# Optimization experiments

Hardware: AMD Instinct MI355X
Metric: run time of the kernel (lower is better)

Reference implementation:

```python
import jax, jax.numpy as jnp
import numpy as np

B, C, H, W = 16, 512, 32, 32
CQ = C // 8  # 64
EPS = 1e-5


def _conv1x1(x, Wt, b=None):
    # x: (B,C,H,W), Wt: (O,C) -> (B,O,H,W)
    y = jnp.einsum('bchw,oc->bohw', x, Wt)
    if b is not None:
        y = y + b[None, :, None, None]
    return y


def setup_inputs() -> dict:
    key = jax.random.key(0)
    ks = jax.random.split(key, 12)
    s = 0.02
    return {
        'rgb':    jax.random.normal(ks[0], (B, C, H, W), jnp.float32),
        'depth':  jax.random.normal(ks[1], (B, C, H, W), jnp.float32),
        'Wq_rgb': jax.random.normal(ks[2], (CQ, C), jnp.float32) * s,
        'bq_rgb': jnp.zeros((CQ,), jnp.float32),
        'Wk_dep': jax.random.normal(ks[3], (CQ, C), jnp.float32) * s,
        'bk_dep': jnp.zeros((CQ,), jnp.float32),
        'Wv_dep': jax.random.normal(ks[4], (C, C), jnp.float32) * s,
        'bv_dep': jnp.zeros((C,), jnp.float32),
        'Wq_dep': jax.random.normal(ks[5], (CQ, C), jnp.float32) * s,
        'bq_dep': jnp.zeros((CQ,), jnp.float32),
        'Wk_rgb': jax.random.normal(ks[6], (CQ, C), jnp.float32) * s,
        'bk_rgb': jnp.zeros((CQ,), jnp.float32),
        'Wv_rgb': jax.random.normal(ks[7], (C, C), jnp.float32) * s,
        'bv_rgb': jnp.zeros((C,), jnp.float32),
        'W_fuse': jax.random.normal(ks[8], (C, 2 * C), jnp.float32) * s,
        'gamma':  jnp.ones((C,), jnp.float32),
        'beta':   jnp.zeros((C,), jnp.float32),
    }


def reference(rgb, depth, Wq_rgb, bq_rgb, Wk_dep, bk_dep, Wv_dep, bv_dep,
              Wq_dep, bq_dep, Wk_rgb, bk_rgb, Wv_rgb, bv_rgb, W_fuse, gamma, beta):
    b, c, h, w = rgb.shape
    hw = h * w
    scale = jnp.asarray(c, rgb.dtype) ** 0.5  # note: full C, as in source

    # RGB attends to depth
    q = _conv1x1(rgb, Wq_rgb, bq_rgb).reshape(b, -1, hw).transpose(0, 2, 1)   # (B,HW,CQ)
    k = _conv1x1(depth, Wk_dep, bk_dep).reshape(b, -1, hw)                    # (B,CQ,HW)
    v = _conv1x1(depth, Wv_dep, bv_dep).reshape(b, -1, hw).transpose(0, 2, 1) # (B,HW,C)
    attn = jax.nn.softmax(jnp.einsum('bnd,bdm->bnm', q, k) / scale, axis=-1)
    rgb_att = jnp.einsum('bnm,bmc->bnc', attn, v).transpose(0, 2, 1).reshape(b, c, h, w)

    # Depth attends to RGB
    q2 = _conv1x1(depth, Wq_dep, bq_dep).reshape(b, -1, hw).transpose(0, 2, 1)
    k2 = _conv1x1(rgb, Wk_rgb, bk_rgb).reshape(b, -1, hw)
    v2 = _conv1x1(rgb, Wv_rgb, bv_rgb).reshape(b, -1, hw).transpose(0, 2, 1)
    attn2 = jax.nn.softmax(jnp.einsum('bnd,bdm->bnm', q2, k2) / scale, axis=-1)
    dep_att = jnp.einsum('bnm,bmc->bnc', attn2, v2).transpose(0, 2, 1).reshape(b, c, h, w)

    cat = jnp.concatenate([rgb_att, dep_att], axis=1)      # (B,2C,H,W)
    fused = jnp.einsum('bchw,oc->bohw', cat, W_fuse)        # 1x1 conv, no bias

    # BatchNorm2d in training mode (batch statistics, biased variance)
    mean = fused.mean(axis=(0, 2, 3))
    var = fused.var(axis=(0, 2, 3))
    normed = (fused - mean[None, :, None, None]) * jax.lax.rsqrt(var + EPS)[None, :, None, None]
    out = normed * gamma[None, :, None, None] + beta[None, :, None, None]
    return jax.nn.relu(out)
```

## Files before the change

### kernel.cpp

```cpp
#include <hip/hip_runtime.h>
#include <math.h>

#define NB 16
#define CC 512
#define CQ 64
#define HWN 1024

typedef float4 f4;
typedef __bf16 bf16x8 __attribute__((ext_vector_type(8)));
typedef float f32x4 __attribute__((ext_vector_type(4)));
typedef __attribute__((ext_vector_type(8))) unsigned short ushort8v;

__device__ __forceinline__ unsigned short f2bf(float f) {
    unsigned int u = __float_as_uint(f);
    u = (u + 0x7fffu + ((u >> 16) & 1u)) >> 16;
    return (unsigned short)u;
}
__device__ __forceinline__ float bf2f(unsigned short u) {
    return __uint_as_float(((unsigned int)u) << 16);
}

__device__ __forceinline__ void gload16(const unsigned short* g, unsigned short* l) {
    __builtin_amdgcn_global_load_lds(
        (const __attribute__((address_space(1))) unsigned int*)g,
        (__attribute__((address_space(3))) unsigned int*)l,
        16, 0, 0);
}

template<int BM, int BN, int BIAS, bool OBF16, int ZSH>
__global__ __launch_bounds__(256)
void mfma_g(const unsigned short* __restrict__ A, long sAlo, long sAhi, int lda,
            const unsigned short* __restrict__ B, long sBlo, long sBhi, int ldb,
            const float* __restrict__ bias, long sBiasHi,
            void* __restrict__ Cout, long sClo, long sChi, int ldc,
            int Ksize, float alpha)
{
    constexpr int MF = BM / 32;
    constexpr int NF = BN / 32;
    constexpr int CA = BM / 32;
    constexpr int CB = BN / 32;
    __shared__ unsigned short As[2][BM * 64];
    __shared__ unsigned short Bs[2][BN * 64];

    const int gx = gridDim.x, gy = gridDim.y;
    int f = blockIdx.x + gx * (blockIdx.y + gy * blockIdx.z);
    const int nwg = gx * gy * gridDim.z;
    f = (f & 7) * (nwg >> 3) + (f >> 3);
    const int bx = f % gx; const int t2 = f / gx;
    const int by = t2 % gy; const int bz = t2 / gy;

    const int zlo = ZSH ? (bz & ((1 << ZSH) - 1)) : 0;
    const int zhi = bz >> ZSH;

    const int t = threadIdx.x, lane = t & 63, wid = t >> 6;
    const int wm = (wid >> 1) * (BM / 2), wn = (wid & 1) * (BN / 2);
    const int m0 = by * BM, n0 = bx * BN;
    const unsigned short* Ab = A + (long)zlo * sAlo + (long)zhi * sAhi;
    const unsigned short* Bb = B + (long)zlo * sBlo + (long)zhi * sBhi;

    const int srow = lane >> 3;
    const int scol = ((lane & 7) ^ srow) << 3;
    const unsigned short* gA[CA]; const unsigned short* gB[CB];
    unsigned short* lA[CA]; unsigned short* lB[CB];
#pragma unroll
    for (int c = 0; c < CA; ++c) {
        const int seg = wid + 4 * c;
        gA[c] = Ab + (long)(m0 + seg * 8 + srow) * lda + scol;
        lA[c] = &As[0][seg * 512];
    }
#pragma unroll
    for (int c = 0; c < CB; ++c) {
        const int seg = wid + 4 * c;
        gB[c] = Bb + (long)(n0 + seg * 8 + srow) * ldb + scol;
        lB[c] = &Bs[0][seg * 512];
    }

    f32x4 acc[MF][NF] = {};
    const int l15 = lane & 15, slot = lane >> 4;

#pragma unroll
    for (int c = 0; c < CA; ++c) gload16(gA[c], lA[c]);
#pragma unroll
    for (int c = 0; c < CB; ++c) gload16(gB[c], lB[c]);
    __syncthreads();

    const int nt = Ksize >> 6;
    int cur = 0;
    for (int tt = 0; tt < nt; ++tt) {
        if (tt + 1 < nt) {
            const int ko = (tt + 1) << 6;
            const int nb = cur ^ 1;
#pragma unroll
            for (int c = 0; c < CA; ++c) gload16(gA[c] + ko, lA[c] + nb * (BM * 64));
#pragma unroll
            for (int c = 0; c < CB; ++c) gload16(gB[c] + ko, lB[c] + nb * (BN * 64));
        }
        bf16x8 alo[MF], ahi[MF], blo[NF], bhi[NF];
#pragma unroll
        for (int i = 0; i < MF; ++i) {
            const int r = wm + i * 16 + l15;
            alo[i] = *(const bf16x8*)&As[cur][r * 64 + ((slot ^ (r & 7)) << 3)];
            ahi[i] = *(const bf16x8*)&As[cur][r * 64 + (((slot + 4) ^ (r & 7)) << 3)];
        }
#pragma unroll
        for (int j = 0; j < NF; ++j) {
            const int r = wn + j * 16 + l15;
            blo[j] = *(const bf16x8*)&Bs[cur][r * 64 + ((slot ^ (r & 7)) << 3)];
            bhi[j] = *(const bf16x8*)&Bs[cur][r * 64 + (((slot + 4) ^ (r & 7)) << 3)];
        }
#pragma unroll
        for (int i = 0; i < MF; ++i)
#pragma unroll
            for (int j = 0; j < NF; ++j) {
                acc[i][j] = __builtin_amdgcn_mfma_f32_16x16x32_bf16(alo[i], blo[j], acc[i][j], 0, 0, 0);
                acc[i][j] = __builtin_amdgcn_mfma_f32_16x16x32_bf16(ahi[i], bhi[j], acc[i][j], 0, 0, 0);
            }
        __syncthreads();
        cur ^= 1;
    }

    unsigned short* C16 = (unsigned short*)Cout + (long)zlo * sClo + (long)zhi * sChi;
    float*          C32 = (float*)Cout + (long)zlo * sClo + (long)zhi * sChi;
    const float* biasb = (BIAS != 0) ? bias + (long)zhi * sBiasHi : nullptr;
    const int r0 = slot << 2;
#pragma unroll
    for (int i = 0; i < MF; ++i) {
#pragma unroll
        for (int r = 0; r < 4; ++r) {
            const int m = m0 + wm + i * 16 + r0 + r;
            const float brow = (BIAS == 1) ? biasb[m] : 0.0f;
#pragma unroll
            for (int j = 0; j < NF; ++j) {
                const int n = n0 + wn + j * 16 + l15;
                const float bb = (BIAS == 2) ? biasb[n] : brow;
                const float o = alpha * (acc[i][j][r] + bb);
                if (OBF16) C16[(long)m * ldc + n] = f2bf(o);
                else       C32[(long)m * ldc + n] = o;
            }
        }
    }
}

__global__ __launch_bounds__(256)
void attn_fused(const unsigned short* __restrict__ QK, unsigned short* __restrict__ Pcat)
{
    __shared__ unsigned short Ss[32][1024];
    const int t = threadIdx.x, lane = t & 63, w = t >> 6;
    const int bx = blockIdx.x, b = blockIdx.y, dir = blockIdx.z;
    const unsigned short* Q = QK + (long)(dir ? b : 16 + b) * 131072;
    const unsigned short* K = QK + (long)(dir ? 16 + b : b) * 131072 + 64;
    const int l15 = lane & 15, kg = (lane >> 4) << 3;

    const long mrow = bx * 32 + (w & 1) * 16 + l15;
    bf16x8 aq0 = *(const bf16x8*)&Q[mrow * 128 + kg];
    bf16x8 aq1 = *(const bf16x8*)&Q[mrow * 128 + 32 + kg];

    const int colbase = (w >> 1) * 512;
    const int rbase = (w & 1) * 16 + (lane >> 4) * 4;
    for (int c = 0; c < 4; ++c) {
        const int n0 = colbase + c * 128;
        bf16x8 bk0[8], bk1[8];
#pragma unroll
        for (int j = 0; j < 8; ++j) {
            const long krow = n0 + j * 16 + l15;
            bk0[j] = *(const bf16x8*)&K[krow * 128 + kg];
            bk1[j] = *(const bf16x8*)&K[krow * 128 + 32 + kg];
        }
#pragma unroll
        for (int j = 0; j < 8; ++j) {
            f32x4 a = {0.f, 0.f, 0.f, 0.f};
            a = __builtin_amdgcn_mfma_f32_16x16x32_bf16(aq0, bk0[j], a, 0, 0, 0);
            a = __builtin_amdgcn_mfma_f32_16x16x32_bf16(aq1, bk1[j], a, 0, 0, 0);
            const int col = n0 + j * 16 + l15;
#pragma unroll
            for (int r = 0; r < 4; ++r)
                Ss[rbase + r][col] = f2bf(a[r]);
        }
    }
    __syncthreads();

    for (int rr = 0; rr < 8; ++rr) {
        const int R = w * 8 + rr;
        ushort8v u0 = *(const ushort8v*)&Ss[R][lane * 8];
        ushort8v u1 = *(const ushort8v*)&Ss[R][512 + lane * 8];
        float v[16];
#pragma unroll
        for (int i = 0; i < 8; ++i) { v[i] = bf2f(u0[i]); v[8 + i] = bf2f(u1[i]); }
        float m = v[0];
#pragma unroll
        for (int i = 1; i < 16; ++i) m = fmaxf(m, v[i]);
#pragma unroll
        for (int off = 32; off; off >>= 1) m = fmaxf(m, __shfl_xor(m, off));
        float s = 0.0f;
#pragma unroll
        for (int i = 0; i < 16; ++i) { v[i] = __expf(v[i] - m); s += v[i]; }
#pragma unroll
        for (int off = 32; off; off >>= 1) s += __shfl_xor(s, off);
        const float inv = 1.0f / s;
        ushort8v o0, o1;
#pragma unroll
        for (int i = 0; i < 8; ++i) { o0[i] = f2bf(v[i] * inv); o1[i] = f2bf(v[8 + i] * inv); }
        unsigned short* dst = Pcat + ((long)(b * 1024 + bx * 32 + R)) * 2048 + dir * 1024 + lane * 8;
        *(ushort8v*)dst = o0;
        *(ushort8v*)(dst + 512) = o1;
    }
}

__global__ __launch_bounds__(256)
void transpose_cvt2(const float* __restrict__ src_dep, const float* __restrict__ src_rgb,
                    unsigned short* __restrict__ dst)
{
    __shared__ float tile[64][65];
    const int t = threadIdx.x;
    const int z = blockIdx.z;
    const float* s = (z < 16 ? src_dep : src_rgb) + (long)(z & 15) * 524288;
    unsigned short* d = dst + (long)z * 524288;
    const int c0 = blockIdx.x << 6, r0 = blockIdx.y << 6;
    const int lr = t >> 4, lc = (t & 15) << 2;
#pragma unroll
    for (int i = 0; i < 4; ++i) {
        f4 v = *(const f4*)(s + (long)(r0 + lr + i * 16) * HWN + c0 + lc);
        *(f4*)&tile[lr + i * 16][lc] = v;
    }
    __syncthreads();
#pragma unroll
    for (int i = 0; i < 4; ++i) {
        const int crow = lr + i * 16;
        ushort4 o;
        o.x = f2bf(tile[lc + 0][crow]);
        o.y = f2bf(tile[lc + 1][crow]);
        o.z = f2bf(tile[lc + 2][crow]);
        o.w = f2bf(tile[lc + 3][crow]);
        *(ushort4*)&d[(long)(c0 + crow) * CC + r0 + lc] = o;
    }
}

__global__ __launch_bounds__(256)
void transpose_cvt(const float* __restrict__ src, unsigned short* __restrict__ dst,
                   int R, int Cn)
{
    __shared__ float tile[64][65];
    const int t = threadIdx.x;
    const int c0 = blockIdx.x << 6, r0 = blockIdx.y << 6;
    const int lr = t >> 4, lc = (t & 15) << 2;
#pragma unroll
    for (int i = 0; i < 4; ++i) {
        f4 v = *(const f4*)(src + (long)(r0 + lr + i * 16) * Cn + c0 + lc);
        *(f4*)&tile[lr + i * 16][lc] = v;
    }
    __syncthreads();
#pragma unroll
    for (int i = 0; i < 4; ++i) {
        const int crow = lr + i * 16;
        ushort4 o;
        o.x = f2bf(tile[lc + 0][crow]);
        o.y = f2bf(tile[lc + 1][crow]);
        o.z = f2bf(tile[lc + 2][crow]);
        o.w = f2bf(tile[lc + 3][crow]);
        *(ushort4*)&dst[(long)(c0 + crow) * R + r0 + lc] = o;
    }
}

__global__ __launch_bounds__(256)
void cvt_flat(const float* __restrict__ src, unsigned short* __restrict__ dst, int n4)
{
    const int i = blockIdx.x * 256 + threadIdx.x;
    if (i < n4) {
        f4 v = ((const f4*)src)[i];
        ushort4 o;
        o.x = f2bf(v.x); o.y = f2bf(v.y); o.z = f2bf(v.z); o.w = f2bf(v.w);
        ((ushort4*)dst)[i] = o;
    }
}

__global__ __launch_bounds__(256)
void prep_wqk(const float* __restrict__ wqd, const float* __restrict__ wkd,
              const float* __restrict__ wqr, const float* __restrict__ wkr,
              unsigned short* __restrict__ dst, float s)
{
    const int i4 = blockIdx.x * 256 + threadIdx.x;
    const int row = i4 >> 7;
    const int seg = row >> 6;
    const float* src = (seg == 0) ? wqd : (seg == 1) ? wkd : (seg == 2) ? wqr : wkr;
    const float sc = (seg & 1) ? 1.0f : s;
    f4 v = ((const f4*)src)[((row & 63) << 7) + (i4 & 127)];
    ushort4 o;
    o.x = f2bf(v.x * sc); o.y = f2bf(v.y * sc); o.z = f2bf(v.z * sc); o.w = f2bf(v.w * sc);
    ((ushort4*)dst)[i4] = o;
}

__global__ __launch_bounds__(256)
void prep_bias(const float* __restrict__ bqd, const float* __restrict__ bkd,
               const float* __restrict__ bqr, const float* __restrict__ bkr,
               float* __restrict__ dst, float s)
{
    const int t = threadIdx.x;
    float v;
    if (t < 64)       v = bqd[t] * s;
    else if (t < 128) v = bkd[t - 64];
    else if (t < 192) v = bqr[t - 128] * s;
    else              v = bkr[t - 192];
    dst[t] = v;
}

__global__ __launch_bounds__(256)
void bfuse_k(const float* __restrict__ Wf, const float* __restrict__ bv1,
             const float* __restrict__ bv2, float* __restrict__ bfuse)
{
    const int o = blockIdx.x, t = threadIdx.x;
    const float* row = Wf + (long)o * 1024;
    float s = row[t] * bv1[t] + row[512 + t] * bv2[t]
            + row[256 + t] * bv1[256 + t] + row[768 + t] * bv2[256 + t];
#pragma unroll
    for (int off = 32; off; off >>= 1) s += __shfl_xor(s, off);
    __shared__ float r[4];
    if ((t & 63) == 0) r[t >> 6] = s;
    __syncthreads();
    if (t == 0) bfuse[o] = r[0] + r[1] + r[2] + r[3];
}

__global__ __launch_bounds__(256)
void bn_stats(const float* __restrict__ fused, float* __restrict__ stats)
{
    const int o = blockIdx.x, t = threadIdx.x;
    float s = 0.0f, s2 = 0.0f;
    for (int b = 0; b < NB; ++b) {
        f4 v = *(const f4*)(fused + ((long)(b * CC + o) << 10) + (t << 2));
        s  += v.x + v.y + v.z + v.w;
        s2 += v.x * v.x + v.y * v.y + v.z * v.z + v.w * v.w;
    }
#pragma unroll
    for (int off = 32; off; off >>= 1) {
        s  += __shfl_xor(s, off);
        s2 += __shfl_xor(s2, off);
    }
    __shared__ float r1[4], r2[4];
    if ((t & 63) == 0) { r1[t >> 6] = s; r2[t >> 6] = s2; }
    __syncthreads();
    if (t == 0) {
        const float S1 = r1[0] + r1[1] + r1[2] + r1[3];
        const float S2 = r2[0] + r2[1] + r2[2] + r2[3];
        const float mean = S1 * (1.0f / 16384.0f);
        const float var  = S2 * (1.0f / 16384.0f) - mean * mean;
        stats[o]      = mean;
        stats[CC + o] = rsqrtf(var + 1e-5f);
    }
}

__global__ __launch_bounds__(256)
void bn_apply(const float* __restrict__ fused, const float* __restrict__ stats,
              const float* __restrict__ gamma, const float* __restrict__ beta,
              float* __restrict__ out)
{
    const long i4 = (long)blockIdx.x * 256 + threadIdx.x;
    f4 v = ((const f4*)fused)[i4];
    const int o = (int)((i4 >> 8) & 511);
    const float is = stats[CC + o];
    const float g  = gamma[o] * is;
    const float bb = beta[o] - stats[o] * g;
    v.x = fmaxf(fmaf(v.x, g, bb), 0.0f);
    v.y = fmaxf(fmaf(v.y, g, bb), 0.0f);
    v.z = fmaxf(fmaf(v.z, g, bb), 0.0f);
    v.w = fmaxf(fmaf(v.w, g, bb), 0.0f);
    ((f4*)out)[i4] = v;
}

static constexpr long B_depT  = 0;
static constexpr long B_rgbT  = 16777216;
static constexpr long B_WvT1  = 33554432;
static constexpr long B_WvT2  = 34078720;
static constexpr long B_Wfb   = 34603008;
static constexpr long B_Wqk   = 35651584;
static constexpr long B_Wc1   = 35913728;
static constexpr long B_Wc2   = 36438016;
static constexpr long B_bfu   = 36962304;
static constexpr long B_bias  = 36964352;
static constexpr long B_QK    = 36966400;
static constexpr long B_Acat  = 45355008;
static constexpr long B_Pcat  = 78909440;
static constexpr long B_fused = 146018304;
static constexpr long B_stats = 179572736;

extern "C" void kernel_launch(void* const* d_in, const int* in_sizes, int n_in,
                              void* d_out, int out_size, void* d_ws, size_t ws_size,
                              hipStream_t stream)
{
    const float* rgb    = (const float*)d_in[0];
    const float* depth  = (const float*)d_in[1];
    const float* Wq_rgb = (const float*)d_in[2];
    const float* bq_rgb = (const float*)d_in[3];
    const float* Wk_dep = (const float*)d_in[4];
    const float* bk_dep = (const float*)d_in[5];
    const float* Wv_dep = (const float*)d_in[6];
    const float* bv_dep = (const float*)d_in[7];
    const float* Wq_dep = (const float*)d_in[8];
    const float* bq_dep = (const float*)d_in[9];
    const float* Wk_rgb = (const float*)d_in[10];
    const float* bk_rgb = (const float*)d_in[11];
    const float* Wv_rgb = (const float*)d_in[12];
    const float* bv_rgb = (const float*)d_in[13];
    const float* W_fuse = (const float*)d_in[14];
    const float* gamma  = (const float*)d_in[15];
    const float* beta   = (const float*)d_in[16];
    char* ws = (char*)d_ws;
    float* out = (float*)d_out;

    const float inv_scale = 0.044194173824159223f;
    dim3 blk(256);

    unsigned short* depT = (unsigned short*)(ws + B_depT);
    unsigned short* WvT1 = (unsigned short*)(ws + B_WvT1);
    unsigned short* WvT2 = (unsigned short*)(ws + B_WvT2);
    unsigned short* Wfb  = (unsigned short*)(ws + B_Wfb);
    unsigned short* Wqk  = (unsigned short*)(ws + B_Wqk);
    unsigned short* Wc1  = (unsigned short*)(ws + B_Wc1);
    float*          bfu  = (float*)(ws + B_bfu);
    float*          bias = (float*)(ws + B_bias);
    unsigned short* QK   = (unsigned short*)(ws + B_QK);
    unsigned short* Acat = (unsigned short*)(ws + B_Acat);
    unsigned short* Pcat = (unsigned short*)(ws + B_Pcat);
    float*          fused= (float*)(ws + B_fused);
    float*          stats= (float*)(ws + B_stats);

    transpose_cvt2<<<dim3(16, 8, 32), blk, 0, stream>>>(depth, rgb, depT);
    transpose_cvt<<<dim3(8, 8, 1), blk, 0, stream>>>(Wv_dep, WvT1, CC, CC);
    transpose_cvt<<<dim3(8, 8, 1), blk, 0, stream>>>(Wv_rgb, WvT2, CC, CC);
    cvt_flat<<<512, blk, 0, stream>>>(W_fuse, Wfb, 131072);
    prep_wqk<<<128, blk, 0, stream>>>(Wq_dep, Wk_dep, Wq_rgb, Wk_rgb, Wqk, inv_scale);
    prep_bias<<<1, blk, 0, stream>>>(bq_dep, bk_dep, bq_rgb, bk_rgb, bias, inv_scale);
    bfuse_k<<<512, blk, 0, stream>>>(W_fuse, bv_dep, bv_rgb, bfu);

    mfma_g<128, 128, 0, true, 0><<<dim3(4, 4, 2), blk, 0, stream>>>(
        Wfb, 0, 512, 1024, WvT1, 0, 262144, 512, nullptr, 0,
        Wc1, 0, 262144, 512, 512, 1.0f);

    mfma_g<128, 64, 2, true, 4><<<dim3(2, 8, 32), blk, 0, stream>>>(
        depT, 524288, 8388608, 512, Wqk, 0, 65536, 512, bias, 128,
        QK, 131072, 2097152, 128, 512, 1.0f);

    mfma_g<128, 128, 0, true, 4><<<dim3(8, 4, 32), blk, 0, stream>>>(
        Wc1, 0, 262144, 512, depT, 524288, 8388608, 512, nullptr, 0,
        Acat, 1048576, 1024, 2048, 512, 1.0f);

    attn_fused<<<dim3(32, NB, 2), blk, 0, stream>>>(QK, Pcat);

    mfma_g<128, 128, 1, false, 4><<<dim3(8, 4, 16), blk, 0, stream>>>(
        Acat, 1048576, 0, 2048, Pcat, 2097152, 0, 2048, bfu, 0,
        fused, 524288, 0, 1024, 2048, 1.0f);

    bn_stats<<<CC, blk, 0, stream>>>(fused, stats);
    bn_apply<<<8192, blk, 0, stream>>>(fused, stats, gamma, beta, out);
}
```

Baseline: 187.9 us.

## Fuse BatchNorm statistics into final GEMM epilogue and simplify attention softmax

The final fuse GEMM now accumulates per-channel sum and sum-of-squares in its epilogue using shuffle reductions and atomicAdds into a zeroed buffer. This replaces the separate bn_stats pass that re-read the whole fused tensor with a tiny finalize kernel. The attention kernel now handles 16 query rows per block, applies exp directly to the logits in fp32 shared memory with an XOR swizzle, and drops the max-subtraction pass and the bf16 staging. The trade-offs are atomic contention, non-deterministic summation order, and a risk of overflow if logits are large, since the softmax is no longer max-stabilised.

```diff
diff --git a/kernel.cpp b/kernel.cpp
--- a/kernel.cpp
+++ b/kernel.cpp
@@ -27,13 +27,13 @@
         16, 0, 0);
 }
 
-template<int BM, int BN, int BIAS, bool OBF16, int ZSH>
+template<int BM, int BN, int BIAS, bool OBF16, int ZSH, bool STATS>
 __global__ __launch_bounds__(256)
 void mfma_g(const unsigned short* __restrict__ A, long sAlo, long sAhi, int lda,
             const unsigned short* __restrict__ B, long sBlo, long sBhi, int ldb,
             const float* __restrict__ bias, long sBiasHi,
             void* __restrict__ Cout, long sClo, long sChi, int ldc,
-            int Ksize, float alpha)
+            int Ksize, float alpha, float* __restrict__ statsAcc)
 {
     constexpr int MF = BM / 32;
     constexpr int NF = BN / 32;
@@ -129,6 +129,7 @@
         for (int r = 0; r < 4; ++r) {
             const int m = m0 + wm + i * 16 + r0 + r;
             const float brow = (BIAS == 1) ? biasb[m] : 0.0f;
+            float ps = 0.0f, ps2 = 0.0f;
 #pragma unroll
             for (int j = 0; j < NF; ++j) {
                 const int n = n0 + wn + j * 16 + l15;
@@ -136,73 +137,93 @@
                 const float o = alpha * (acc[i][j][r] + bb);
                 if (OBF16) C16[(long)m * ldc + n] = f2bf(o);
                 else       C32[(long)m * ldc + n] = o;
+                if (STATS) { ps += o; ps2 += o * o; }
             }
-        }
-    }
-}
-
-__global__ __launch_bounds__(256)
-void attn_fused(const unsigned short* __restrict__ QK, unsigned short* __restrict__ Pcat)
-{
-    __shared__ unsigned short Ss[32][1024];
+            if (STATS) {
+#pragma unroll
+                for (int off = 8; off; off >>= 1) {
+                    ps  += __shfl_xor(ps, off);
+                    ps2 += __shfl_xor(ps2, off);
+                }
+                if (l15 == 0) {
+                    atomicAdd(&statsAcc[m], ps);
+                    atomicAdd(&statsAcc[CC + m], ps2);
+                }
+            }
+        }
+    }
+}
+
+__global__ __launch_bounds__(256)
+void attn_fused2(const unsigned short* __restrict__ QK, unsigned short* __restrict__ Pcat)
+{
+    __shared__ float Es[16 * 1024];
     const int t = threadIdx.x, lane = t & 63, w = t >> 6;
     const int bx = blockIdx.x, b = blockIdx.y, dir = blockIdx.z;
     const unsigned short* Q = QK + (long)(dir ? b : 16 + b) * 131072;
     const unsigned short* K = QK + (long)(dir ? 16 + b : b) * 131072 + 64;
-    const int l15 = lane & 15, kg = (lane >> 4) << 3;
-
-    const long mrow = bx * 32 + (w & 1) * 16 + l15;
+    const int l15 = lane & 15, slot = lane >> 4, kg = slot << 3;
+
+    const long mrow = (long)bx * 16 + l15;
     bf16x8 aq0 = *(const bf16x8*)&Q[mrow * 128 + kg];
     bf16x8 aq1 = *(const bf16x8*)&Q[mrow * 128 + 32 + kg];
 
-    const int colbase = (w >> 1) * 512;
-    const int rbase = (w & 1) * 16 + (lane >> 4) * 4;
+    const int colbase = w << 8;
+    const int rbase = slot << 2;
+#pragma unroll
     for (int c = 0; c < 4; ++c) {
-        const int n0 = colbase + c * 128;
-        bf16x8 bk0[8], bk1[8];
-#pragma unroll
-        for (int j = 0; j < 8; ++j) {
-            const long krow = n0 + j * 16 + l15;
+        const int n0 = colbase + (c << 6);
+        bf16x8 bk0[4], bk1[4];
+#pragma unroll
+        for (int j = 0; j < 4; ++j) {
+            const long krow = n0 + (j << 4) + l15;
             bk0[j] = *(const bf16x8*)&K[krow * 128 + kg];
             bk1[j] = *(const bf16x8*)&K[krow * 128 + 32 + kg];
         }
 #pragma unroll
-        for (int j = 0; j < 8; ++j) {
+        for (int j = 0; j < 4; ++j) {
             f32x4 a = {0.f, 0.f, 0.f, 0.f};
             a = __builtin_amdgcn_mfma_f32_16x16x32_bf16(aq0, bk0[j], a, 0, 0, 0);
             a = __builtin_amdgcn_mfma_f32_16x16x32_bf16(aq1, bk1[j], a, 0, 0, 0);
-            const int col = n0 + j * 16 + l15;
-#pragma unroll
-            for (int r = 0; r < 4; ++r)
-                Ss[rbase + r][col] = f2bf(a[r]);
+            const int col = n0 + (j << 4) + l15;
+#pragma unroll
+            for (int r = 0; r < 4; ++r) {
+                const int row = rbase + r;
+                Es[(row << 10) + (col ^ (row << 2))] = __expf(a[r]);
+            }
         }
     }
     __syncthreads();
 
-    for (int rr = 0; rr < 8; ++rr) {
-        const int R = w * 8 + rr;
-        ushort8v u0 = *(const ushort8v*)&Ss[R][lane * 8];
-        ushort8v u1 = *(const ushort8v*)&Ss[R][512 + lane * 8];
-        float v[16];
-#pragma unroll
-        for (int i = 0; i < 8; ++i) { v[i] = bf2f(u0[i]); v[8 + i] = bf2f(u1[i]); }
-        float m = v[0];
-#pragma unroll
-        for (int i = 1; i < 16; ++i) m = fmaxf(m, v[i]);
-#pragma unroll
-        for (int off = 32; off; off >>= 1) m = fmaxf(m, __shfl_xor(m, off));
-        float s = 0.0f;
-#pragma unroll
-        for (int i = 0; i < 16; ++i) { v[i] = __expf(v[i] - m); s += v[i]; }
+#pragma unroll
+    for (int rr = 0; rr < 4; ++rr) {
+        const int R = (w << 2) + rr;
+        const int base = R << 10, sw = R << 2;
+        const int c4 = lane << 2;
+        f4 v0 = *(const f4*)&Es[base + ((c4 +   0) ^ sw)];
+        f4 v1 = *(const f4*)&Es[base + ((c4 + 256) ^ sw)];
+        f4 v2 = *(const f4*)&Es[base + ((c4 + 512) ^ sw)];
+        f4 v3 = *(const f4*)&Es[base + ((c4 + 768) ^ sw)];
+        float s = (v0.x + v0.y + v0.z + v0.w) + (v1.x + v1.y + v1.z + v1.w)
+                + (v2.x + v2.y + v2.z + v2.w) + (v3.x + v3.y + v3.z + v3.w);
 #pragma unroll
         for (int off = 32; off; off >>= 1) s += __shfl_xor(s, off);
         const float inv = 1.0f / s;
-        ushort8v o0, o1;
-#pragma unroll
-        for (int i = 0; i < 8; ++i) { o0[i] = f2bf(v[i] * inv); o1[i] = f2bf(v[8 + i] * inv); }
-        unsigned short* dst = Pcat + ((long)(b * 1024 + bx * 32 + R)) * 2048 + dir * 1024 + lane * 8;
-        *(ushort8v*)dst = o0;
-        *(ushort8v*)(dst + 512) = o1;
+        unsigned short* dst = Pcat + ((long)(b * 1024 + bx * 16 + R)) * 2048
+                            + dir * 1024 + (lane << 2);
+        ushort4 o;
+        o.x = f2bf(v0.x * inv); o.y = f2bf(v0.y * inv);
+        o.z = f2bf(v0.z * inv); o.w = f2bf(v0.w * inv);
+        *(ushort4*)(dst +   0) = o;
+        o.x = f2bf(v1.x * inv); o.y = f2bf(v1.y * inv);
+        o.z = f2bf(v1.z * inv); o.w = f2bf(v1.w * inv);
+        *(ushort4*)(dst + 256) = o;
+        o.x = f2bf(v2.x * inv); o.y = f2bf(v2.y * inv);
+        o.z = f2bf(v2.z * inv); o.w = f2bf(v2.w * inv);
+        *(ushort4*)(dst + 512) = o;
+        o.x = f2bf(v3.x * inv); o.y = f2bf(v3.y * inv);
+        o.z = f2bf(v3.z * inv); o.w = f2bf(v3.w * inv);
+        *(ushort4*)(dst + 768) = o;
     }
 }
 
@@ -319,32 +340,14 @@
     if (t == 0) bfuse[o] = r[0] + r[1] + r[2] + r[3];
 }
 
-__global__ __launch_bounds__(256)
-void bn_stats(const float* __restrict__ fused, float* __restrict__ stats)
-{
-    const int o = blockIdx.x, t = threadIdx.x;
-    float s = 0.0f, s2 = 0.0f;
-    for (int b = 0; b < NB; ++b) {
-        f4 v = *(const f4*)(fused + ((long)(b * CC + o) << 10) + (t << 2));
-        s  += v.x + v.y + v.z + v.w;
-        s2 += v.x * v.x + v.y * v.y + v.z * v.z + v.w * v.w;
-    }
-#pragma unroll
-    for (int off = 32; off; off >>= 1) {
-        s  += __shfl_xor(s, off);
-        s2 += __shfl_xor(s2, off);
-    }
-    __shared__ float r1[4], r2[4];
-    if ((t & 63) == 0) { r1[t >> 6] = s; r2[t >> 6] = s2; }
-    __syncthreads();
-    if (t == 0) {
-        const float S1 = r1[0] + r1[1] + r1[2] + r1[3];
-        const float S2 = r2[0] + r2[1] + r2[2] + r2[3];
-        const float mean = S1 * (1.0f / 16384.0f);
-        const float var  = S2 * (1.0f / 16384.0f) - mean * mean;
-        stats[o]      = mean;
-        stats[CC + o] = rsqrtf(var + 1e-5f);
-    }
+__global__ __launch_bounds__(512)
+void bn_finalize(const float* __restrict__ S12, float* __restrict__ stats)
+{
+    const int o = threadIdx.x;
+    const float mean = S12[o] * (1.0f / 16384.0f);
+    const float var  = S12[CC + o] * (1.0f / 16384.0f) - mean * mean;
+    stats[o]      = mean;
+    stats[CC + o] = rsqrtf(var + 1e-5f);
 }
 
 __global__ __launch_bounds__(256)
@@ -372,7 +375,6 @@
 static constexpr long B_Wfb   = 34603008;
 static constexpr long B_Wqk   = 35651584;
 static constexpr long B_Wc1   = 35913728;
-static constexpr long B_Wc2   = 36438016;
 static constexpr long B_bfu   = 36962304;
 static constexpr long B_bias  = 36964352;
 static constexpr long B_QK    = 36966400;
@@ -380,6 +382,7 @@
 static constexpr long B_Pcat  = 78909440;
 static constexpr long B_fused = 146018304;
 static constexpr long B_stats = 179572736;
+static constexpr long B_S12   = 179576832;
 
 extern "C" void kernel_launch(void* const* d_in, const int* in_sizes, int n_in,
                               void* d_out, int out_size, void* d_ws, size_t ws_size,
@@ -421,7 +424,9 @@
     unsigned short* Pcat = (unsigned short*)(ws + B_Pcat);
     float*          fused= (float*)(ws + B_fused);
     float*          stats= (float*)(ws + B_stats);
-
+    float*          S12  = (float*)(ws + B_S12);
+
+    hipMemsetAsync(S12, 0, 1024 * sizeof(float), stream);
     transpose_cvt2<<<dim3(16, 8, 32), blk, 0, stream>>>(depth, rgb, depT);
     transpose_cvt<<<dim3(8, 8, 1), blk, 0, stream>>>(Wv_dep, WvT1, CC, CC);
     transpose_cvt<<<dim3(8, 8, 1), blk, 0, stream>>>(Wv_rgb, WvT2, CC, CC);
@@ -430,24 +435,24 @@
     prep_bias<<<1, blk, 0, stream>>>(bq_dep, bk_dep, bq_rgb, bk_rgb, bias, inv_scale);
     bfuse_k<<<512, blk, 0, stream>>>(W_fuse, bv_dep, bv_rgb, bfu);
 
-    mfma_g<128, 128, 0, true, 0><<<dim3(4, 4, 2), blk, 0, stream>>>(
+    mfma_g<128, 128, 0, true, 0, false><<<dim3(4, 4, 2), blk, 0, stream>>>(
         Wfb, 0, 512, 1024, WvT1, 0, 262144, 512, nullptr, 0,
-        Wc1, 0, 262144, 512, 512, 1.0f);
-
-    mfma_g<128, 64, 2, true, 4><<<dim3(2, 8, 32), blk, 0, stream>>>(
+        Wc1, 0, 262144, 512, 512, 1.0f, nullptr);
+
+    mfma_g<128, 64, 2, true, 4, false><<<dim3(2, 8, 32), blk, 0, stream>>>(
         depT, 524288, 8388608, 512, Wqk, 0, 65536, 512, bias, 128,
-        QK, 131072, 2097152, 128, 512, 1.0f);
-
-    mfma_g<128, 128, 0, true, 4><<<dim3(8, 4, 32), blk, 0, stream>>>(
+        QK, 131072, 2097152, 128, 512, 1.0f, nullptr);
+
+    mfma_g<128, 128, 0, true, 4, false><<<dim3(8, 4, 32), blk, 0, stream>>>(
         Wc1, 0, 262144, 512, depT, 524288, 8388608, 512, nullptr, 0,
-        Acat, 1048576, 1024, 2048, 512, 1.0f);
-
-    attn_fused<<<dim3(32, NB, 2), blk, 0, stream>>>(QK, Pcat);
-
-    mfma_g<128, 128, 1, false, 4><<<dim3(8, 4, 16), blk, 0, stream>>>(
+        Acat, 1048576, 1024, 2048, 512, 1.0f, nullptr);
+
+    attn_fused2<<<dim3(64, NB, 2), blk, 0, stream>>>(QK, Pcat);
+
+    mfma_g<128, 128, 1, false, 4, true><<<dim3(8, 4, 16), blk, 0, stream>>>(
         Acat, 1048576, 0, 2048, Pcat, 2097152, 0, 2048, bfu, 0,
-        fused, 524288, 0, 1024, 2048, 1.0f);
-
-    bn_stats<<<CC, blk, 0, stream>>>(fused, stats);
+        fused, 524288, 0, 1024, 2048, 1.0f, S12);
+
+    bn_finalize<<<1, 512, 0, stream>>>(S12, stats);
     bn_apply<<<8192, blk, 0, stream>>>(fused, stats, gamma, beta, out);
 }
```

Measured after the change: 212.3 us. +13.0%, slower.
